# Performance work log

Measured on AMD Instinct MI355X. Metric: run time of the kernel, lower is better.

Reference implementation:

```python
import jax, jax.numpy as jnp
import numpy as np

EPS = 1e-6  # matches module eps


def _l2_norm_ch(t):
    # normalize over channel axis (dim=-2), matching torch l2_norm helper
    return t / jnp.linalg.norm(t, axis=-2, keepdims=True)


def setup_inputs() -> dict:
    key = jax.random.key(0)
    ks = jax.random.split(key, 8)
    B, C, H, W = 8, 256, 128, 128
    m = C // 2  # scale=2
    x = jax.random.normal(ks[0], (B, C, H, W), dtype=jnp.float32)
    Wq = jax.random.normal(ks[1], (m, C), dtype=jnp.float32) * 0.05
    bq = jax.random.normal(ks[2], (m,), dtype=jnp.float32) * 0.05
    Wk = jax.random.normal(ks[3], (m, C), dtype=jnp.float32) * 0.05
    bk = jax.random.normal(ks[4], (m,), dtype=jnp.float32) * 0.05
    Wv = jax.random.normal(ks[5], (C, C), dtype=jnp.float32) * 0.05
    bv = jax.random.normal(ks[6], (C,), dtype=jnp.float32) * 0.05
    # gamma is a zero-init nn.Parameter in the module; use a random scalar so
    # the output is non-trivial for correctness checking.
    gamma = jax.random.normal(ks[7], (1,), dtype=jnp.float32)
    return {"x": x, "Wq": Wq, "bq": bq, "Wk": Wk, "bk": bk, "Wv": Wv, "bv": bv, "gamma": gamma}


def reference(x, Wq, bq, Wk, bk, Wv, bv, gamma):
    B, C, H, W = x.shape  # module names these (batch, channels, width, height)
    N = H * W
    xf = x.reshape(B, C, N)
    # 1x1 convs == per-pixel linear maps over channels
    Q = jnp.einsum('mc,bcn->bmn', Wq, xf) + bq[None, :, None]   # [B, m, N]
    K = jnp.einsum('mc,bcn->bmn', Wk, xf) + bk[None, :, None]   # [B, m, N]
    V = jnp.einsum('oc,bcn->bon', Wv, xf) + bv[None, :, None]   # [B, C, N]
    Qn = _l2_norm_ch(Q).transpose(0, 2, 1)  # [B, N, m]
    Kn = _l2_norm_ch(K)                      # [B, m, N]
    Ksum = jnp.sum(Kn, axis=-1) + EPS        # [B, m]
    tailor = 1.0 / (N + jnp.einsum('bnm,bm->bn', Qn, Ksum))  # [B, N]
    vsum = jnp.sum(V, axis=-1)                                # [B, C]
    matrix = jnp.einsum('bmn,bcn->bmc', Kn, V)                # [B, m, C]
    matrix_sum = vsum[:, :, None] + jnp.einsum('bnm,bmc->bcn', Qn, matrix)  # [B, C, N]
    weight_value = matrix_sum * tailor[:, None, :]
    return (gamma * weight_value).reshape(B, C, H, W)
```

## Files before the change

kernel.cpp:

```cpp
#include <hip/hip_runtime.h>
#include <math.h>

typedef unsigned short ushort_t;
typedef __attribute__((ext_vector_type(4))) float f32x4;
typedef __attribute__((ext_vector_type(8))) short short8;

#define MFMA16(a, b, c) __builtin_amdgcn_mfma_f32_16x16x32_bf16((a), (b), (c), 0, 0, 0)

constexpr int kB = 8;
constexpr int kC = 256;
constexpr int kM = 128;
constexpr int kN = 16384;

constexpr size_t kOffSp   = 0;
constexpr size_t kOffS    = 16777216;
constexpr size_t kOffKsum = 17825792;
constexpr size_t kOffXsum = 17829888;
constexpr size_t kOffVsum = 17838080;
constexpr size_t kOffWkb  = 17846272;
constexpr size_t kOffWqb  = 17911808;
constexpr size_t kOffMatT = 17977344;

__device__ __forceinline__ ushort_t f2bf(float f) {
  union { float f; unsigned u; } v; v.f = f;
  unsigned r = v.u + 0x7fffu + ((v.u >> 16) & 1u);
  return (ushort_t)(r >> 16);
}
__device__ __forceinline__ float bf2f(ushort_t h) {
  union { float f; unsigned u; } v; v.u = ((unsigned)h) << 16;
  return v.f;
}

__device__ __forceinline__ void sync_lds() {
  __atomic_signal_fence(__ATOMIC_SEQ_CST);
  __builtin_amdgcn_s_waitcnt(0xc07f);
  __builtin_amdgcn_s_barrier();
  __atomic_signal_fence(__ATOMIC_SEQ_CST);
}

__global__ void k0_init(const float* __restrict__ Wq, const float* __restrict__ Wk,
                        float* __restrict__ ws_f, ushort_t* __restrict__ Wkb,
                        ushort_t* __restrict__ Wqb) {
  int i = blockIdx.x * 256 + threadIdx.x;
  float4 z = {0.f, 0.f, 0.f, 0.f};
  float4* sp4 = (float4*)ws_f;
#pragma unroll
  for (int j = 0; j < 4; ++j) sp4[i + j * 262144] = z;
  if (i < 3072) ws_f[4456448 + i] = 0.0f;
  if (i < kM * kC) {
    Wkb[i] = f2bf(Wk[i]);
    Wqb[i] = f2bf(Wq[i]);
  }
}

__global__ __launch_bounds__(512, 2)
void k1_acc(const float* __restrict__ x, const float* __restrict__ bk,
            const ushort_t* __restrict__ Wkb, float* __restrict__ Sp,
            float* __restrict__ Ksum, float* __restrict__ xsum) {
  __shared__ __align__(16) ushort_t xb_n[256][40];
  __shared__ __align__(16) ushort_t xb_t[32][256];
  __shared__ __align__(16) ushort_t knb[128][40];
  __shared__ __align__(16) float red[32][12];

  const int t = threadIdx.x;
  const int b = blockIdx.y;
  const int lane = t & 63, w = t >> 6, quad = lane >> 4, l16 = lane & 15;
  const int r8 = t >> 3;
  const int px0 = 4 * (t & 7);
  const int key01 = (((px0 >> 1)) & 7) << 3;
  const int key23 = key01 ^ 8;
  const int rk = ((l16 >> 1) & 7) << 3;

  float bk_r[4];
#pragma unroll
  for (int r = 0; r < 4; ++r) bk_r[r] = bk[16 * w + 4 * quad + r];

  f32x4 accS[16];
#pragma unroll
  for (int ct = 0; ct < 16; ++ct) accS[ct] = (f32x4){0.f, 0.f, 0.f, 0.f};
  float ksump[4] = {0.f, 0.f, 0.f, 0.f};
  float xs_p[4] = {0.f, 0.f, 0.f, 0.f};

  const float* xg = x + ((size_t)(b * kC) + r8) * kN + blockIdx.x * 256 + px0;

  float4 bufA[4], bufB[4];
#pragma unroll
  for (int p = 0; p < 4; ++p)
    bufA[p] = *(const float4*)(xg + (size_t)p * 64 * kN);

  auto step = [&](int ti, float4 (&cur)[4], float4 (&nxt)[4]) {
    sync_lds();
    if (ti < 7) {
#pragma unroll
      for (int p = 0; p < 4; ++p)
        nxt[p] = *(const float4*)(xg + (size_t)p * 64 * kN + (ti + 1) * 32);
    }
#pragma unroll
    for (int p = 0; p < 4; ++p) {
      float4 v = cur[p];
      const int rp = 64 * p + r8;
      xs_p[p] += v.x + v.y + v.z + v.w;
      ushort_t u0 = f2bf(v.x), u1 = f2bf(v.y), u2 = f2bf(v.z), u3 = f2bf(v.w);
      uint2 pk;
      pk.x = (unsigned)u0 | ((unsigned)u1 << 16);
      pk.y = (unsigned)u2 | ((unsigned)u3 << 16);
      *(uint2*)&xb_n[rp][px0] = pk;
      xb_t[px0 + 0][rp ^ key01] = u0;
      xb_t[px0 + 1][rp ^ key01] = u1;
      xb_t[px0 + 2][rp ^ key23] = u2;
      xb_t[px0 + 3][rp ^ key23] = u3;
    }
    sync_lds();

    f32x4 acc1[2] = {{0.f, 0.f, 0.f, 0.f}, {0.f, 0.f, 0.f, 0.f}};
    const ushort_t* wkbase = Wkb + (16 * w + l16) * 256 + quad * 8;
#pragma unroll
    for (int ks = 0; ks < 8; ++ks) {
      short8 a = *(const short8*)(wkbase + ks * 32);
      short8 b0 = *(const short8*)&xb_t[l16][(ks * 32 + quad * 8) ^ rk];
      short8 b1 = *(const short8*)&xb_t[16 + l16][(ks * 32 + quad * 8) ^ rk];
      acc1[0] = MFMA16(a, b0, acc1[0]);
      acc1[1] = MFMA16(a, b1, acc1[1]);
    }
    float k0v[4], k1v[4];
    float ssq0 = 0.f, ssq1 = 0.f;
#pragma unroll
    for (int r = 0; r < 4; ++r) {
      k0v[r] = acc1[0][r] + bk_r[r];
      k1v[r] = acc1[1][r] + bk_r[r];
      ssq0 += k0v[r] * k0v[r];
      ssq1 += k1v[r] * k1v[r];
    }
    ssq0 += __shfl_xor(ssq0, 16); ssq0 += __shfl_xor(ssq0, 32);
    ssq1 += __shfl_xor(ssq1, 16); ssq1 += __shfl_xor(ssq1, 32);
    if (quad == 0) { red[l16][w] = ssq0; red[16 + l16][w] = ssq1; }
    sync_lds();

    f32x4 ra = *(const f32x4*)&red[l16][0];
    f32x4 rb = *(const f32x4*)&red[l16][4];
    f32x4 rc = *(const f32x4*)&red[16 + l16][0];
    f32x4 rd = *(const f32x4*)&red[16 + l16][4];
    const float iv0 = rsqrtf(ra[0] + ra[1] + ra[2] + ra[3] + rb[0] + rb[1] + rb[2] + rb[3]);
    const float iv1 = rsqrtf(rc[0] + rc[1] + rc[2] + rc[3] + rd[0] + rd[1] + rd[2] + rd[3]);
#pragma unroll
    for (int r = 0; r < 4; ++r) {
      float kn0 = k0v[r] * iv0, kn1 = k1v[r] * iv1;
      ksump[r] += kn0 + kn1;
      knb[16 * w + 4 * quad + r][l16] = f2bf(kn0);
      knb[16 * w + 4 * quad + r][16 + l16] = f2bf(kn1);
    }
    __builtin_amdgcn_s_waitcnt(0xc07f);

    short8 a2 = *(const short8*)&knb[16 * w + l16][quad * 8];
#pragma unroll
    for (int ct = 0; ct < 16; ++ct) {
      short8 b2 = *(const short8*)&xb_n[ct * 16 + l16][quad * 8];
      accS[ct] = MFMA16(a2, b2, accS[ct]);
    }
  };

  for (int ti = 0; ti < 8; ti += 2) {
    step(ti, bufA, bufB);
    step(ti + 1, bufB, bufA);
  }

  float* Sb = Sp + ((size_t)(b * 16) + (blockIdx.x & 15)) * kM * kC;
  if (((blockIdx.x >> 4) & 1) == 0) {
#pragma unroll
    for (int ct = 0; ct < 16; ++ct)
#pragma unroll
      for (int r = 0; r < 4; ++r)
        atomicAdd(&Sb[(16 * w + 4 * quad + r) * 256 + ct * 16 + l16], accS[ct][r]);
  } else {
#pragma unroll
    for (int ct = 15; ct >= 0; --ct)
#pragma unroll
      for (int r = 0; r < 4; ++r)
        atomicAdd(&Sb[(16 * w + 4 * quad + r) * 256 + ct * 16 + l16], accS[ct][r]);
  }
#pragma unroll
  for (int r = 0; r < 4; ++r) {
    float v = ksump[r];
    v += __shfl_xor(v, 1); v += __shfl_xor(v, 2);
    v += __shfl_xor(v, 4); v += __shfl_xor(v, 8);
    if (l16 == 0) atomicAdd(&Ksum[b * kM + 16 * w + 4 * quad + r], v);
  }
#pragma unroll
  for (int p = 0; p < 4; ++p) {
    float v = xs_p[p];
    v += __shfl_xor(v, 1); v += __shfl_xor(v, 2); v += __shfl_xor(v, 4);
    if ((t & 7) == 0) atomicAdd(&xsum[b * kC + 64 * p + r8], v);
  }
}

__global__ __launch_bounds__(256)
void k1_reduce(const float* __restrict__ Sp, float* __restrict__ S) {
  const int idx = blockIdx.x * 256 + threadIdx.x;
  const int b = idx >> 15, rem = idx & 32767;
  const float* base = Sp + (((size_t)b * 16) << 15) + rem;
  float s = 0.f;
#pragma unroll
  for (int p = 0; p < 16; ++p) s += base[(size_t)p << 15];
  S[idx] = s;
}

__global__ __launch_bounds__(256, 4)
void k2_matrix(const float* __restrict__ S, const float* __restrict__ Ksum,
               const float* __restrict__ xsum, const float* __restrict__ Wv,
               const float* __restrict__ bv, ushort_t* __restrict__ matT,
               float* __restrict__ vsum) {
  const int t = threadIdx.x;
  const int lane = t & 63, w = t >> 6, quad = lane >> 4, l16 = lane & 15;
  const int bx = blockIdx.x;
  const int b = bx >> 5, ct = (bx >> 1) & 15, mt = bx & 1;
  const int c0 = ct * 16;
  const int m0 = mt * 64 + w * 16;

  const float* arow = Wv + (size_t)(c0 + l16) * 256 + quad * 8;
  const float* brow = S + ((size_t)b * kM + m0 + l16) * 256 + quad * 8;
  const bool do_vsum = (mt == 0) && (w == 0);
  const float* xsb = xsum + b * kC + quad * 8;

  f32x4 acc = (f32x4){0.f, 0.f, 0.f, 0.f};
  float vdot = 0.f;

#pragma unroll
  for (int ks = 0; ks < 8; ++ks) {
    float4 a0 = *(const float4*)(arow + ks * 32);
    float4 a1 = *(const float4*)(arow + ks * 32 + 4);
    float4 b0 = *(const float4*)(brow + ks * 32);
    float4 b1 = *(const float4*)(brow + ks * 32 + 4);
    float av[8] = {a0.x, a0.y, a0.z, a0.w, a1.x, a1.y, a1.z, a1.w};
    float bw[8] = {b0.x, b0.y, b0.z, b0.w, b1.x, b1.y, b1.z, b1.w};
    if (do_vsum) {
      float4 x0 = *(const float4*)(xsb + ks * 32);
      float4 x1 = *(const float4*)(xsb + ks * 32 + 4);
      vdot += av[0] * x0.x + av[1] * x0.y + av[2] * x0.z + av[3] * x0.w +
              av[4] * x1.x + av[5] * x1.y + av[6] * x1.z + av[7] * x1.w;
    }
    short8 ah, al, bh, bl;
#pragma unroll
    for (int i = 0; i < 8; ++i) {
      ushort_t h = f2bf(av[i]);
      ah[i] = (short)h;
      al[i] = (short)f2bf(av[i] - bf2f(h));
      ushort_t g = f2bf(bw[i]);
      bh[i] = (short)g;
      bl[i] = (short)f2bf(bw[i] - bf2f(g));
    }
    acc = MFMA16(ah, bh, acc);
    acc = MFMA16(ah, bl, acc);
    acc = MFMA16(al, bh, acc);
  }

  const float ksm = Ksum[b * kM + m0 + l16];
  float4 bv4 = *(const float4*)(bv + c0 + quad * 4);
  float bvv[4] = {bv4.x, bv4.y, bv4.z, bv4.w};
#pragma unroll
  for (int r = 0; r < 4; ++r) {
    const int c = c0 + 4 * quad + r;
    matT[((size_t)b * kC + c) * kM + m0 + l16] = f2bf(acc[r] + ksm * bvv[r]);
  }
  if (do_vsum) {
    vdot += __shfl_xor(vdot, 16);
    vdot += __shfl_xor(vdot, 32);
    if (quad == 0)
      vsum[b * kC + c0 + l16] = vdot + 16384.f * bv[c0 + l16];
  }
}

__global__ __launch_bounds__(512, 2)
void k3_out(const float* __restrict__ x, const float* __restrict__ bq,
            const ushort_t* __restrict__ Wqb, const ushort_t* __restrict__ matT,
            const float* __restrict__ Ksum, const float* __restrict__ vsum,
            const float* __restrict__ gamma, float* __restrict__ out) {
  __shared__ __align__(16) ushort_t xb_t[32][256];
  __shared__ __align__(16) ushort_t qnb[32][136];
  __shared__ __align__(16) float red[32][12];
  __shared__ __align__(16) float red2[32][12];

  const int t = threadIdx.x;
  const int b = blockIdx.y;
  const int lane = t & 63, w = t >> 6, quad = lane >> 4, l16 = lane & 15;
  const int r8 = t >> 3;
  const int px0 = 4 * (t & 7);
  const int key01 = (((px0 >> 1)) & 7) << 3;
  const int key23 = key01 ^ 8;
  const int rk = ((l16 >> 1) & 7) << 3;
  const float gm = gamma[0];

  float bq_r[4], ks_r[4], vs_r[2][4];
#pragma unroll
  for (int r = 0; r < 4; ++r) {
    bq_r[r] = bq[16 * w + 4 * quad + r];
    ks_r[r] = Ksum[b * kM + 16 * w + 4 * quad + r] + 1e-6f;
  }
#pragma unroll
  for (int mi = 0; mi < 2; ++mi)
#pragma unroll
    for (int r = 0; r < 4; ++r)
      vs_r[mi][r] = vsum[b * kC + (2 * w + mi) * 16 + 4 * quad + r];

  const float* xg = x + ((size_t)(b * kC) + r8) * kN + blockIdx.x * 256 + px0;

  float4 bufA[4], bufB[4];
#pragma unroll
  for (int p = 0; p < 4; ++p)
    bufA[p] = *(const float4*)(xg + (size_t)p * 64 * kN);

  auto step = [&](int ti, float4 (&cur)[4], float4 (&nxt)[4]) {
    const int n0 = blockIdx.x * 256 + ti * 32;
    sync_lds();
    if (ti < 7) {
#pragma unroll
      for (int p = 0; p < 4; ++p)
        nxt[p] = *(const float4*)(xg + (size_t)p * 64 * kN + (ti + 1) * 32);
    }
#pragma unroll
    for (int p = 0; p < 4; ++p) {
      float4 v = cur[p];
      const int rp = 64 * p + r8;
      xb_t[px0 + 0][rp ^ key01] = f2bf(v.x);
      xb_t[px0 + 1][rp ^ key01] = f2bf(v.y);
      xb_t[px0 + 2][rp ^ key23] = f2bf(v.z);
      xb_t[px0 + 3][rp ^ key23] = f2bf(v.w);
    }
    sync_lds();

    f32x4 acc1[2] = {{0.f, 0.f, 0.f, 0.f}, {0.f, 0.f, 0.f, 0.f}};
    const ushort_t* wqbase = Wqb + (16 * w + l16) * 256 + quad * 8;
#pragma unroll
    for (int ks = 0; ks < 8; ++ks) {
      short8 a = *(const short8*)(wqbase + ks * 32);
      short8 b0 = *(const short8*)&xb_t[l16][(ks * 32 + quad * 8) ^ rk];
      short8 b1 = *(const short8*)&xb_t[16 + l16][(ks * 32 + quad * 8) ^ rk];
      acc1[0] = MFMA16(a, b0, acc1[0]);
      acc1[1] = MFMA16(a, b1, acc1[1]);
    }
    float q0v[4], q1v[4];
    float ssq0 = 0.f, ssq1 = 0.f, dot0 = 0.f, dot1 = 0.f;
#pragma unroll
    for (int r = 0; r < 4; ++r) {
      q0v[r] = acc1[0][r] + bq_r[r];
      q1v[r] = acc1[1][r] + bq_r[r];
      ssq0 += q0v[r] * q0v[r]; ssq1 += q1v[r] * q1v[r];
      dot0 += q0v[r] * ks_r[r]; dot1 += q1v[r] * ks_r[r];
    }
    ssq0 += __shfl_xor(ssq0, 16); ssq0 += __shfl_xor(ssq0, 32);
    ssq1 += __shfl_xor(ssq1, 16); ssq1 += __shfl_xor(ssq1, 32);
    dot0 += __shfl_xor(dot0, 16); dot0 += __shfl_xor(dot0, 32);
    dot1 += __shfl_xor(dot1, 16); dot1 += __shfl_xor(dot1, 32);
    if (quad == 0) {
      red[l16][w] = ssq0;  red[16 + l16][w] = ssq1;
      red2[l16][w] = dot0; red2[16 + l16][w] = dot1;
    }
    sync_lds();
    f32x4 ra = *(const f32x4*)&red[l16][0];
    f32x4 rb = *(const f32x4*)&red[l16][4];
    f32x4 rc = *(const f32x4*)&red[16 + l16][0];
    f32x4 rd = *(const f32x4*)&red[16 + l16][4];
    f32x4 da = *(const f32x4*)&red2[l16][0];
    f32x4 db = *(const f32x4*)&red2[l16][4];
    f32x4 dc = *(const f32x4*)&red2[16 + l16][0];
    f32x4 dd = *(const f32x4*)&red2[16 + l16][4];
    const float iv0 = rsqrtf(ra[0] + ra[1] + ra[2] + ra[3] + rb[0] + rb[1] + rb[2] + rb[3]);
    const float iv1 = rsqrtf(rc[0] + rc[1] + rc[2] + rc[3] + rd[0] + rd[1] + rd[2] + rd[3]);
    const float d0 = da[0] + da[1] + da[2] + da[3] + db[0] + db[1] + db[2] + db[3];
    const float d1 = dc[0] + dc[1] + dc[2] + dc[3] + dd[0] + dd[1] + dd[2] + dd[3];
    const float tl0 = 1.f / (16384.f + d0 * iv0);
    const float tl1 = 1.f / (16384.f + d1 * iv1);
    {
      ushort_t q0b[4], q1b[4];
#pragma unroll
      for (int r = 0; r < 4; ++r) {
        q0b[r] = f2bf(q0v[r] * iv0);
        q1b[r] = f2bf(q1v[r] * iv1);
      }
      uint2 p0, p1;
      p0.x = (unsigned)q0b[0] | ((unsigned)q0b[1] << 16);
      p0.y = (unsigned)q0b[2] | ((unsigned)q0b[3] << 16);
      p1.x = (unsigned)q1b[0] | ((unsigned)q1b[1] << 16);
      p1.y = (unsigned)q1b[2] | ((unsigned)q1b[3] << 16);
      *(uint2*)&qnb[l16][16 * w + 4 * quad] = p0;
      *(uint2*)&qnb[16 + l16][16 * w + 4 * quad] = p1;
    }
    sync_lds();

    f32x4 accO[2][2];
#pragma unroll
    for (int mi = 0; mi < 2; ++mi)
#pragma unroll
      for (int nt = 0; nt < 2; ++nt) accO[mi][nt] = (f32x4){0.f, 0.f, 0.f, 0.f};
    const ushort_t* mrow0 = matT + ((size_t)b * kC + (2 * w) * 16 + l16) * kM + quad * 8;
    const ushort_t* mrow1 = mrow0 + 16 * kM;
#pragma unroll
    for (int ks = 0; ks < 4; ++ks) {
      short8 b0 = *(const short8*)&qnb[l16][ks * 32 + quad * 8];
      short8 b1 = *(const short8*)&qnb[16 + l16][ks * 32 + quad * 8];
      short8 a0 = *(const short8*)(mrow0 + ks * 32);
      short8 a1 = *(const short8*)(mrow1 + ks * 32);
      accO[0][0] = MFMA16(a0, b0, accO[0][0]);
      accO[0][1] = MFMA16(a0, b1, accO[0][1]);
      accO[1][0] = MFMA16(a1, b0, accO[1][0]);
      accO[1][1] = MFMA16(a1, b1, accO[1][1]);
    }
#pragma unroll
    for (int mi = 0; mi < 2; ++mi) {
#pragma unroll
      for (int r = 0; r < 4; ++r) {
        const int c = (2 * w + mi) * 16 + 4 * quad + r;
        size_t base = ((size_t)(b * kC + c)) * kN + n0;
        out[base + l16] = gm * tl0 * (vs_r[mi][r] + accO[mi][0][r]);
        out[base + 16 + l16] = gm * tl1 * (vs_r[mi][r] + accO[mi][1][r]);
      }
    }
  };

  for (int ti = 0; ti < 8; ti += 2) {
    step(ti, bufA, bufB);
    step(ti + 1, bufB, bufA);
  }
}

extern "C" void kernel_launch(void* const* d_in, const int* in_sizes, int n_in,
                              void* d_out, int out_size, void* d_ws, size_t ws_size,
                              hipStream_t stream) {
  (void)in_sizes; (void)n_in; (void)out_size; (void)ws_size;
  const float* x     = (const float*)d_in[0];
  const float* Wq    = (const float*)d_in[1];
  const float* bq    = (const float*)d_in[2];
  const float* Wk    = (const float*)d_in[3];
  const float* bk    = (const float*)d_in[4];
  const float* Wv    = (const float*)d_in[5];
  const float* bv    = (const float*)d_in[6];
  const float* gamma = (const float*)d_in[7];
  float* out = (float*)d_out;

  char* wsb = (char*)d_ws;
  float*    Sp   = (float*)(wsb + kOffSp);
  float*    S    = (float*)(wsb + kOffS);
  float*    Ksum = (float*)(wsb + kOffKsum);
  float*    xsum = (float*)(wsb + kOffXsum);
  float*    vsum = (float*)(wsb + kOffVsum);
  ushort_t* Wkb  = (ushort_t*)(wsb + kOffWkb);
  ushort_t* Wqb  = (ushort_t*)(wsb + kOffWqb);
  ushort_t* matT = (ushort_t*)(wsb + kOffMatT);

  k0_init<<<1024, 256, 0, stream>>>(Wq, Wk, (float*)wsb, Wkb, Wqb);
  k1_acc<<<dim3(64, 8), 512, 0, stream>>>(x, bk, Wkb, Sp, Ksum, xsum);
  k1_reduce<<<1024, 256, 0, stream>>>(Sp, S);
  k2_matrix<<<256, 256, 0, stream>>>(S, Ksum, xsum, Wv, bv, matT, vsum);
  k3_out<<<dim3(64, 8), 512, 0, stream>>>(x, bq, Wqb, matT, Ksum, vsum, gamma, out);
}
```

Baseline: 343.3 us.

## Split K projection from S accumulation and stage bf16 x copy for reuse

```diff
diff --git a/kernel.cpp b/kernel.cpp
--- a/kernel.cpp
+++ b/kernel.cpp
@@ -12,14 +12,16 @@
 constexpr int kM = 128;
 constexpr int kN = 16384;
 
-constexpr size_t kOffSp   = 0;
-constexpr size_t kOffS    = 16777216;
-constexpr size_t kOffKsum = 17825792;
-constexpr size_t kOffXsum = 17829888;
-constexpr size_t kOffVsum = 17838080;
-constexpr size_t kOffWkb  = 17846272;
-constexpr size_t kOffWqb  = 17911808;
-constexpr size_t kOffMatT = 17977344;
+constexpr size_t kOffS    = 0;
+constexpr size_t kOffMatF = 1048576;
+constexpr size_t kOffKsum = 2097152;
+constexpr size_t kOffXsum = 2101248;
+constexpr size_t kOffVsum = 2109440;
+constexpr size_t kOffWkb  = 2117632;
+constexpr size_t kOffWqb  = 2183168;
+constexpr size_t kOffMatT = 2248704;
+constexpr size_t kOffKn   = 2772992;
+constexpr size_t kOffXb16 = 36327424;
 
 __device__ __forceinline__ ushort_t f2bf(float f) {
   union { float f; unsigned u; } v; v.f = f;
@@ -42,22 +44,20 @@
                         float* __restrict__ ws_f, ushort_t* __restrict__ Wkb,
                         ushort_t* __restrict__ Wqb) {
   int i = blockIdx.x * 256 + threadIdx.x;
-  float4 z = {0.f, 0.f, 0.f, 0.f};
-  float4* sp4 = (float4*)ws_f;
-#pragma unroll
-  for (int j = 0; j < 4; ++j) sp4[i + j * 262144] = z;
-  if (i < 3072) ws_f[4456448 + i] = 0.0f;
+  ws_f[i] = 0.0f;
+  ws_f[i + 262144] = 0.0f;
+  if (i < 3072) ws_f[524288 + i] = 0.0f;
   if (i < kM * kC) {
     Wkb[i] = f2bf(Wk[i]);
     Wqb[i] = f2bf(Wq[i]);
   }
 }
 
-__global__ __launch_bounds__(512, 2)
-void k1_acc(const float* __restrict__ x, const float* __restrict__ bk,
-            const ushort_t* __restrict__ Wkb, float* __restrict__ Sp,
-            float* __restrict__ Ksum, float* __restrict__ xsum) {
-  __shared__ __align__(16) ushort_t xb_n[256][40];
+__global__ __launch_bounds__(512, 6)
+void k1a_proj(const float* __restrict__ x, const float* __restrict__ bk,
+              const ushort_t* __restrict__ Wkb, ushort_t* __restrict__ KnG,
+              ushort_t* __restrict__ xb16, float* __restrict__ Ksum,
+              float* __restrict__ xsum) {
   __shared__ __align__(16) ushort_t xb_t[32][256];
   __shared__ __align__(16) ushort_t knb[128][40];
   __shared__ __align__(16) float red[32][12];
@@ -67,44 +67,34 @@
   const int lane = t & 63, w = t >> 6, quad = lane >> 4, l16 = lane & 15;
   const int r8 = t >> 3;
   const int px0 = 4 * (t & 7);
-  const int key01 = (((px0 >> 1)) & 7) << 3;
+  const int key01 = ((px0 >> 1) & 7) << 3;
   const int key23 = key01 ^ 8;
   const int rk = ((l16 >> 1) & 7) << 3;
+  const int krow = 16 * w + (lane >> 2);
+  const int kch = (lane & 3) * 8;
 
   float bk_r[4];
 #pragma unroll
   for (int r = 0; r < 4; ++r) bk_r[r] = bk[16 * w + 4 * quad + r];
-
-  f32x4 accS[16];
-#pragma unroll
-  for (int ct = 0; ct < 16; ++ct) accS[ct] = (f32x4){0.f, 0.f, 0.f, 0.f};
   float ksump[4] = {0.f, 0.f, 0.f, 0.f};
   float xs_p[4] = {0.f, 0.f, 0.f, 0.f};
 
   const float* xg = x + ((size_t)(b * kC) + r8) * kN + blockIdx.x * 256 + px0;
-
-  float4 bufA[4], bufB[4];
-#pragma unroll
-  for (int p = 0; p < 4; ++p)
-    bufA[p] = *(const float4*)(xg + (size_t)p * 64 * kN);
-
-  auto step = [&](int ti, float4 (&cur)[4], float4 (&nxt)[4]) {
-    sync_lds();
-    if (ti < 7) {
-#pragma unroll
-      for (int p = 0; p < 4; ++p)
-        nxt[p] = *(const float4*)(xg + (size_t)p * 64 * kN + (ti + 1) * 32);
-    }
+  ushort_t* xw = xb16 + ((size_t)(b * kC) + r8) * kN + blockIdx.x * 256 + px0;
+
+  for (int ti = 0; ti < 8; ++ti) {
+    const int n0 = blockIdx.x * 256 + ti * 32;
+    sync_lds();
 #pragma unroll
     for (int p = 0; p < 4; ++p) {
-      float4 v = cur[p];
+      float4 v = *(const float4*)(xg + (size_t)p * 64 * kN + ti * 32);
       const int rp = 64 * p + r8;
       xs_p[p] += v.x + v.y + v.z + v.w;
       ushort_t u0 = f2bf(v.x), u1 = f2bf(v.y), u2 = f2bf(v.z), u3 = f2bf(v.w);
       uint2 pk;
       pk.x = (unsigned)u0 | ((unsigned)u1 << 16);
       pk.y = (unsigned)u2 | ((unsigned)u3 << 16);
-      *(uint2*)&xb_n[rp][px0] = pk;
+      *(uint2*)(xw + (size_t)p * 64 * kN + ti * 32) = pk;
       xb_t[px0 + 0][rp ^ key01] = u0;
       xb_t[px0 + 1][rp ^ key01] = u1;
       xb_t[px0 + 2][rp ^ key23] = u2;
@@ -150,34 +140,10 @@
       knb[16 * w + 4 * quad + r][16 + l16] = f2bf(kn1);
     }
     __builtin_amdgcn_s_waitcnt(0xc07f);
-
-    short8 a2 = *(const short8*)&knb[16 * w + l16][quad * 8];
-#pragma unroll
-    for (int ct = 0; ct < 16; ++ct) {
-      short8 b2 = *(const short8*)&xb_n[ct * 16 + l16][quad * 8];
-      accS[ct] = MFMA16(a2, b2, accS[ct]);
-    }
-  };
-
-  for (int ti = 0; ti < 8; ti += 2) {
-    step(ti, bufA, bufB);
-    step(ti + 1, bufB, bufA);
-  }
-
-  float* Sb = Sp + ((size_t)(b * 16) + (blockIdx.x & 15)) * kM * kC;
-  if (((blockIdx.x >> 4) & 1) == 0) {
-#pragma unroll
-    for (int ct = 0; ct < 16; ++ct)
-#pragma unroll
-      for (int r = 0; r < 4; ++r)
-        atomicAdd(&Sb[(16 * w + 4 * quad + r) * 256 + ct * 16 + l16], accS[ct][r]);
-  } else {
-#pragma unroll
-    for (int ct = 15; ct >= 0; --ct)
-#pragma unroll
-      for (int r = 0; r < 4; ++r)
-        atomicAdd(&Sb[(16 * w + 4 * quad + r) * 256 + ct * 16 + l16], accS[ct][r]);
-  }
+    short8 kv8 = *(const short8*)&knb[krow][kch];
+    *(short8*)(KnG + ((size_t)b * kM + krow) * kN + n0 + kch) = kv8;
+  }
+
 #pragma unroll
   for (int r = 0; r < 4; ++r) {
     float v = ksump[r];
@@ -193,51 +159,76 @@
   }
 }
 
-__global__ __launch_bounds__(256)
-void k1_reduce(const float* __restrict__ Sp, float* __restrict__ S) {
-  const int idx = blockIdx.x * 256 + threadIdx.x;
-  const int b = idx >> 15, rem = idx & 32767;
-  const float* base = Sp + (((size_t)b * 16) << 15) + rem;
-  float s = 0.f;
-#pragma unroll
-  for (int p = 0; p < 16; ++p) s += base[(size_t)p << 15];
-  S[idx] = s;
+__global__ __launch_bounds__(512, 4)
+void k1b_S(const ushort_t* __restrict__ KnG, const ushort_t* __restrict__ xb16,
+           float* __restrict__ S) {
+  const int t = threadIdx.x;
+  const int b = blockIdx.y;
+  const int lane = t & 63, w = t >> 6, quad = lane >> 4, l16 = lane & 15;
+  const int px0 = blockIdx.x * 256;
+
+  f32x4 acc[16];
+#pragma unroll
+  for (int ct = 0; ct < 16; ++ct) acc[ct] = (f32x4){0.f, 0.f, 0.f, 0.f};
+
+  const ushort_t* arow = KnG + ((size_t)b * kM + 16 * w + l16) * kN + px0 + quad * 8;
+  const ushort_t* brow = xb16 + ((size_t)b * kC + l16) * kN + px0 + quad * 8;
+
+#pragma unroll 2
+  for (int kk = 0; kk < 8; ++kk) {
+    short8 a2 = *(const short8*)(arow + kk * 32);
+#pragma unroll
+    for (int ct = 0; ct < 16; ++ct) {
+      short8 b2 = *(const short8*)(brow + (size_t)ct * 16 * kN + kk * 32);
+      acc[ct] = MFMA16(a2, b2, acc[ct]);
+    }
+  }
+
+  float* Sb = S + (size_t)b * kM * kC;
+#pragma unroll
+  for (int ct = 0; ct < 16; ++ct)
+#pragma unroll
+    for (int r = 0; r < 4; ++r)
+      atomicAdd(&Sb[(16 * w + 4 * quad + r) * 256 + ct * 16 + l16], acc[ct][r]);
 }
 
 __global__ __launch_bounds__(256, 4)
-void k2_matrix(const float* __restrict__ S, const float* __restrict__ Ksum,
-               const float* __restrict__ xsum, const float* __restrict__ Wv,
-               const float* __restrict__ bv, ushort_t* __restrict__ matT,
-               float* __restrict__ vsum) {
+void k2_matrix(const float* __restrict__ S, const float* __restrict__ Wv,
+               const float* __restrict__ xsum, const float* __restrict__ bv,
+               float* __restrict__ matF, float* __restrict__ vsum) {
+  const int bx = blockIdx.x;
   const int t = threadIdx.x;
+  if (bx >= 1024) {
+    const int b = bx - 1024;
+    const float4* wr = (const float4*)(Wv + (size_t)t * 256);
+    const float4* xs = (const float4*)(xsum + b * 256);
+    float v = 0.f;
+#pragma unroll 8
+    for (int i = 0; i < 64; ++i) {
+      float4 a = wr[i], xx = xs[i];
+      v += a.x * xx.x + a.y * xx.y + a.z * xx.z + a.w * xx.w;
+    }
+    vsum[b * 256 + t] = v + 16384.f * bv[t];
+    return;
+  }
   const int lane = t & 63, w = t >> 6, quad = lane >> 4, l16 = lane & 15;
-  const int bx = blockIdx.x;
-  const int b = bx >> 5, ct = (bx >> 1) & 15, mt = bx & 1;
+  const int b = bx >> 7, rr_ = bx & 127;
+  const int ct = rr_ >> 3, mt = (rr_ >> 2) & 1, kq = rr_ & 3;
   const int c0 = ct * 16;
   const int m0 = mt * 64 + w * 16;
 
-  const float* arow = Wv + (size_t)(c0 + l16) * 256 + quad * 8;
-  const float* brow = S + ((size_t)b * kM + m0 + l16) * 256 + quad * 8;
-  const bool do_vsum = (mt == 0) && (w == 0);
-  const float* xsb = xsum + b * kC + quad * 8;
+  const float* arow = Wv + (size_t)(c0 + l16) * 256 + kq * 64 + quad * 8;
+  const float* brow = S + ((size_t)b * kM + m0 + l16) * 256 + kq * 64 + quad * 8;
 
   f32x4 acc = (f32x4){0.f, 0.f, 0.f, 0.f};
-  float vdot = 0.f;
-
-#pragma unroll
-  for (int ks = 0; ks < 8; ++ks) {
+#pragma unroll
+  for (int ks = 0; ks < 2; ++ks) {
     float4 a0 = *(const float4*)(arow + ks * 32);
     float4 a1 = *(const float4*)(arow + ks * 32 + 4);
     float4 b0 = *(const float4*)(brow + ks * 32);
     float4 b1 = *(const float4*)(brow + ks * 32 + 4);
     float av[8] = {a0.x, a0.y, a0.z, a0.w, a1.x, a1.y, a1.z, a1.w};
     float bw[8] = {b0.x, b0.y, b0.z, b0.w, b1.x, b1.y, b1.z, b1.w};
-    if (do_vsum) {
-      float4 x0 = *(const float4*)(xsb + ks * 32);
-      float4 x1 = *(const float4*)(xsb + ks * 32 + 4);
-      vdot += av[0] * x0.x + av[1] * x0.y + av[2] * x0.z + av[3] * x0.w +
-              av[4] * x1.x + av[5] * x1.y + av[6] * x1.z + av[7] * x1.w;
-    }
     short8 ah, al, bh, bl;
 #pragma unroll
     for (int i = 0; i < 8; ++i) {
@@ -252,25 +243,21 @@
     acc = MFMA16(ah, bl, acc);
     acc = MFMA16(al, bh, acc);
   }
-
-  const float ksm = Ksum[b * kM + m0 + l16];
-  float4 bv4 = *(const float4*)(bv + c0 + quad * 4);
-  float bvv[4] = {bv4.x, bv4.y, bv4.z, bv4.w};
-#pragma unroll
-  for (int r = 0; r < 4; ++r) {
-    const int c = c0 + 4 * quad + r;
-    matT[((size_t)b * kC + c) * kM + m0 + l16] = f2bf(acc[r] + ksm * bvv[r]);
-  }
-  if (do_vsum) {
-    vdot += __shfl_xor(vdot, 16);
-    vdot += __shfl_xor(vdot, 32);
-    if (quad == 0)
-      vsum[b * kC + c0 + l16] = vdot + 16384.f * bv[c0 + l16];
-  }
+#pragma unroll
+  for (int r = 0; r < 4; ++r)
+    atomicAdd(&matF[((size_t)b * kC + c0 + 4 * quad + r) * kM + m0 + l16], acc[r]);
+}
+
+__global__ __launch_bounds__(256)
+void k2b_cast(const float* __restrict__ matF, const float* __restrict__ Ksum,
+              const float* __restrict__ bv, ushort_t* __restrict__ matT) {
+  const int idx = blockIdx.x * 256 + threadIdx.x;
+  const int m = idx & 127, c = (idx >> 7) & 255, b = idx >> 15;
+  matT[idx] = f2bf(matF[idx] + Ksum[b * 128 + m] * bv[c]);
 }
 
 __global__ __launch_bounds__(512, 2)
-void k3_out(const float* __restrict__ x, const float* __restrict__ bq,
+void k3_out(const ushort_t* __restrict__ xb16, const float* __restrict__ bq,
             const ushort_t* __restrict__ Wqb, const ushort_t* __restrict__ matT,
             const float* __restrict__ Ksum, const float* __restrict__ vsum,
             const float* __restrict__ gamma, float* __restrict__ out) {
@@ -284,7 +271,7 @@
   const int lane = t & 63, w = t >> 6, quad = lane >> 4, l16 = lane & 15;
   const int r8 = t >> 3;
   const int px0 = 4 * (t & 7);
-  const int key01 = (((px0 >> 1)) & 7) << 3;
+  const int key01 = ((px0 >> 1) & 7) << 3;
   const int key23 = key01 ^ 8;
   const int rk = ((l16 >> 1) & 7) << 3;
   const float gm = gamma[0];
@@ -301,29 +288,29 @@
     for (int r = 0; r < 4; ++r)
       vs_r[mi][r] = vsum[b * kC + (2 * w + mi) * 16 + 4 * quad + r];
 
-  const float* xg = x + ((size_t)(b * kC) + r8) * kN + blockIdx.x * 256 + px0;
-
-  float4 bufA[4], bufB[4];
+  const ushort_t* xg = xb16 + ((size_t)(b * kC) + r8) * kN + blockIdx.x * 256 + px0;
+
+  uint2 bufA[4], bufB[4];
 #pragma unroll
   for (int p = 0; p < 4; ++p)
-    bufA[p] = *(const float4*)(xg + (size_t)p * 64 * kN);
-
-  auto step = [&](int ti, float4 (&cur)[4], float4 (&nxt)[4]) {
+    bufA[p] = *(const uint2*)(xg + (size_t)p * 64 * kN);
+
+  auto step = [&](int ti, uint2 (&cur)[4], uint2 (&nxt)[4]) {
     const int n0 = blockIdx.x * 256 + ti * 32;
     sync_lds();
     if (ti < 7) {
 #pragma unroll
       for (int p = 0; p < 4; ++p)
-        nxt[p] = *(const float4*)(xg + (size_t)p * 64 * kN + (ti + 1) * 32);
+        nxt[p] = *(const uint2*)(xg + (size_t)p * 64 * kN + (ti + 1) * 32);
     }
 #pragma unroll
     for (int p = 0; p < 4; ++p) {
-      float4 v = cur[p];
+      uint2 v = cur[p];
       const int rp = 64 * p + r8;
-      xb_t[px0 + 0][rp ^ key01] = f2bf(v.x);
-      xb_t[px0 + 1][rp ^ key01] = f2bf(v.y);
-      xb_t[px0 + 2][rp ^ key23] = f2bf(v.z);
-      xb_t[px0 + 3][rp ^ key23] = f2bf(v.w);
+      xb_t[px0 + 0][rp ^ key01] = (ushort_t)(v.x & 0xffffu);
+      xb_t[px0 + 1][rp ^ key01] = (ushort_t)(v.x >> 16);
+      xb_t[px0 + 2][rp ^ key23] = (ushort_t)(v.y & 0xffffu);
+      xb_t[px0 + 3][rp ^ key23] = (ushort_t)(v.y >> 16);
     }
     sync_lds();
 
@@ -437,18 +424,21 @@
   float* out = (float*)d_out;
 
   char* wsb = (char*)d_ws;
-  float*    Sp   = (float*)(wsb + kOffSp);
   float*    S    = (float*)(wsb + kOffS);
+  float*    matF = (float*)(wsb + kOffMatF);
   float*    Ksum = (float*)(wsb + kOffKsum);
   float*    xsum = (float*)(wsb + kOffXsum);
   float*    vsum = (float*)(wsb + kOffVsum);
   ushort_t* Wkb  = (ushort_t*)(wsb + kOffWkb);
   ushort_t* Wqb  = (ushort_t*)(wsb + kOffWqb);
   ushort_t* matT = (ushort_t*)(wsb + kOffMatT);
+  ushort_t* KnG  = (ushort_t*)(wsb + kOffKn);
+  ushort_t* xb16 = (ushort_t*)(wsb + kOffXb16);
 
   k0_init<<<1024, 256, 0, stream>>>(Wq, Wk, (float*)wsb, Wkb, Wqb);
-  k1_acc<<<dim3(64, 8), 512, 0, stream>>>(x, bk, Wkb, Sp, Ksum, xsum);
-  k1_reduce<<<1024, 256, 0, stream>>>(Sp, S);
-  k2_matrix<<<256, 256, 0, stream>>>(S, Ksum, xsum, Wv, bv, matT, vsum);
-  k3_out<<<dim3(64, 8), 512, 0, stream>>>(x, bq, Wqb, matT, Ksum, vsum, gamma, out);
-}
+  k1a_proj<<<dim3(64, 8), 512, 0, stream>>>(x, bk, Wkb, KnG, xb16, Ksum, xsum);
+  k1b_S<<<dim3(64, 8), 512, 0, stream>>>(KnG, xb16, S);
+  k2_matrix<<<1032, 256, 0, stream>>>(S, Wv, xsum, bv, matF, vsum);
+  k2b_cast<<<1024, 256, 0, stream>>>(matF, Ksum, bv, matT);
+  k3_out<<<dim3(64, 8), 512, 0, stream>>>(xb16, bq, Wqb, matT, Ksum, vsum, gamma, out);
+}
```

New measurement: 508.7 us. 1.48x slower.
